# Kernel optimization log

Hardware: AMD Instinct MI355X
Metric: run time of the kernel (lower is better)

Reference implementation:

```python
import jax, jax.numpy as jnp
import numpy as np

WS = 4      # window size (hardcoded in original forward)
NH = 2      # num_head (module-level constant in original)


def _ln(x, g, b):
    mu = jnp.mean(x, axis=-1, keepdims=True)
    var = jnp.mean((x - mu) ** 2, axis=-1, keepdims=True)
    return (x - mu) * jax.lax.rsqrt(var + 1e-5) * g + b


def _img_to_win(img):
    # [B,H,W,D] -> [B, nW, WS*WS, D]  (matches F.unfold + reshape/transpose)
    B, H, W, D = img.shape
    s = H // WS
    x = img.reshape(B, s, WS, s, WS, D).transpose(0, 1, 3, 2, 4, 5)
    return x.reshape(B, s * s, WS * WS, D)


def _win_to_img(w):
    # [B, nW, WS*WS, D] -> [B,H,W,D]  (matches window2image)
    B, nW, P, D = w.shape
    s = int(np.sqrt(nW))
    x = w.reshape(B, s, s, WS, WS, D).transpose(0, 1, 3, 2, 4, 5)
    return x.reshape(B, s * WS, s * WS, D)


def _mhsa(x, wqkv, bqkv, wo, bo):
    # x: [B, S, D]; note: the original ignores additive_mask, so none is applied
    B, S, D = x.shape
    d = D // NH
    qkv = x @ wqkv.T + bqkv
    q, k, v = jnp.split(qkv, 3, axis=-1)
    q = q.reshape(B, S, NH, d).transpose(0, 2, 1, 3)
    k = k.reshape(B, S, NH, d).transpose(0, 2, 1, 3)
    v = v.reshape(B, S, NH, d).transpose(0, 2, 1, 3)
    p = jax.nn.softmax(jnp.einsum('bhqd,bhkd->bhqk', q, k) / np.sqrt(d).astype(np.float32), axis=-1)
    o = jnp.einsum('bhqk,bhkd->bhqd', p, v).transpose(0, 2, 1, 3).reshape(B, S, D)
    return o @ wo.T + bo


def _gelu(x):
    return jax.nn.gelu(x, approximate=False)


def setup_inputs() -> dict:
    key = jax.random.key(0)
    D = 128
    ks = jax.random.split(key, 16)
    w = lambda k, shp: (jax.random.normal(k, shp, dtype=jnp.float32) * 0.02)
    inp = {
        'x': jax.random.normal(ks[0], (8, 16384, D), dtype=jnp.float32),
        'ln1_g': jnp.ones((D,), jnp.float32), 'ln1_b': jnp.zeros((D,), jnp.float32),
        'ln2_g': jnp.ones((D,), jnp.float32), 'ln2_b': jnp.zeros((D,), jnp.float32),
        'ln3_g': jnp.ones((D,), jnp.float32), 'ln3_b': jnp.zeros((D,), jnp.float32),
        'ln4_g': jnp.ones((D,), jnp.float32), 'ln4_b': jnp.zeros((D,), jnp.float32),
        'qkv1_w': w(ks[1], (3 * D, D)), 'qkv1_b': jnp.zeros((3 * D,), jnp.float32),
        'out1_w': w(ks[2], (D, D)),     'out1_b': jnp.zeros((D,), jnp.float32),
        'qkv2_w': w(ks[3], (3 * D, D)), 'qkv2_b': jnp.zeros((3 * D,), jnp.float32),
        'out2_w': w(ks[4], (D, D)),     'out2_b': jnp.zeros((D,), jnp.float32),
        'mlp1_w1': w(ks[5], (4 * D, D)), 'mlp1_b1': jnp.zeros((4 * D,), jnp.float32),
        'mlp1_w2': w(ks[6], (D, 4 * D)), 'mlp1_b2': jnp.zeros((D,), jnp.float32),
        'mlp2_w1': w(ks[7], (4 * D, D)), 'mlp2_b1': jnp.zeros((4 * D,), jnp.float32),
        'mlp2_w2': w(ks[8], (D, 4 * D)), 'mlp2_b2': jnp.zeros((D,), jnp.float32),
    }
    return inp


def reference(x, ln1_g, ln1_b, ln2_g, ln2_b, ln3_g, ln3_b, ln4_g, ln4_b,
              qkv1_w, qkv1_b, out1_w, out1_b, qkv2_w, qkv2_b, out2_w, out2_b,
              mlp1_w1, mlp1_b1, mlp1_w2, mlp1_b2, mlp2_w1, mlp2_b1, mlp2_w2, mlp2_b2):
    B, N, D = x.shape
    H = int(np.sqrt(N))
    # --- W-MSA branch ---
    x1 = _ln(x, ln1_g, ln1_b)
    wins = _img_to_win(x1.reshape(B, H, H, D))            # [B,nW,P,D]
    nW, P = wins.shape[1], wins.shape[2]
    a1 = _mhsa(wins.reshape(B * nW, P, D), qkv1_w, qkv1_b, out1_w, out1_b)
    # original: input.long() -> truncate toward zero, detached; residual adds
    # window-order flattening (plain reshape, NOT window2image)
    res1 = jax.lax.stop_gradient(jnp.trunc(x)) + a1.reshape(B, N, D)
    h = _gelu(_ln(res1, ln2_g, ln2_b) @ mlp1_w1.T + mlp1_b1)
    h = _gelu(h @ mlp1_w2.T + mlp1_b2)
    out1 = h + res1
    # --- SW-MSA branch ---
    w2 = _ln(out1, ln3_g, ln3_b).reshape(B, nW, P, D)     # plain reshape (window order)
    img = jnp.roll(_win_to_img(w2), (-WS // 2, -WS // 2), axis=(1, 2))
    a2 = _mhsa(_img_to_win(img).reshape(B * nW, P, D), qkv2_w, qkv2_b, out2_w, out2_b)
    img2 = jnp.roll(_win_to_img(a2.reshape(B, nW, P, D)), (WS // 2, WS // 2), axis=(1, 2))
    res2 = out1 + _img_to_win(img2).reshape(B, N, D)      # plain reshape again
    h2 = _gelu(_ln(res2, ln4_g, ln4_b) @ mlp2_w1.T + mlp2_b1)
    h2 = _gelu(h2 @ mlp2_w2.T + mlp2_b2)
    out2 = h2 + res2
    return out2.reshape(B, nW, P, D)
```

## Files before the change

kernel.cpp:

```cpp
#include <hip/hip_runtime.h>
#include <hip/hip_bf16.h>
#include <string.h>


typedef unsigned short u16;
typedef unsigned int   u32;
typedef __attribute__((ext_vector_type(8))) short bf16x8;
typedef __attribute__((ext_vector_type(4))) float f32x4;

#define MFMA(a,b,c) __builtin_amdgcn_mfma_f32_16x16x32_bf16(a,b,c,0,0,0)

__device__ __forceinline__ u16 f2bf(float x) {
    __hip_bfloat16 h = __float2bfloat16(x);
    u16 r; memcpy(&r, &h, 2); return r;
}
__device__ __forceinline__ u32 pack2(float lo, float hi) {
    __hip_bfloat162 h = __float22bfloat162_rn(make_float2(lo, hi));
    u32 r; memcpy(&r, &h, 4); return r;
}
__device__ __forceinline__ float gelu_fast(float x) {
    float t = x * fmaf(x * x, 0.044715f, 1.0f);
    float e = __builtin_amdgcn_exp2f(-2.3022078f * t);
    return x * __builtin_amdgcn_rcpf(1.0f + e);
}
__device__ __forceinline__ bf16x8 ldsfrag(const u16* base, int byte) {
    return *(const bf16x8*)((const char*)base + byte);
}
__device__ __forceinline__ bf16x8 ldg8(const u16* __restrict__ p) {
    return *(const bf16x8*)p;
}
template <int BRANCH>
__device__ __forceinline__ int src_index(int wg, int tok) {
    int win = (wg << 2) + (tok >> 4), p = tok & 15;
    int r = ((win >> 5) << 2) | (p >> 2);
    int c = ((win & 31) << 2) | (p & 3);
    if (BRANCH == 1) return (r << 7) | c;
    int r2 = (r + 2) & 127, c2 = (c + 2) & 127;
    return ((((r2 >> 2) << 5) | (c2 >> 2)) << 4) | ((r2 & 3) << 2) | (c2 & 3);
}

__global__ __launch_bounds__(256)
void cvt_weights(const float* __restrict__ qkv1, const float* __restrict__ o1,
                 const float* __restrict__ w11,  const float* __restrict__ w12,
                 const float* __restrict__ qkv2, const float* __restrict__ o2,
                 const float* __restrict__ w21,  const float* __restrict__ w22,
                 u16* __restrict__ dst)
{
    int e = (blockIdx.x * 256 + threadIdx.x) * 8;
    const float* src; int off;
    if      (e < 49152)  { src = qkv1; off = 0; }
    else if (e < 65536)  { src = o1;   off = 49152; }
    else if (e < 131072) { src = w11;  off = 65536; }
    else if (e < 196608) { src = w12;  off = 131072; }
    else if (e < 245760) { src = qkv2; off = 196608; }
    else if (e < 262144) { src = o2;   off = 245760; }
    else if (e < 327680) { src = w21;  off = 262144; }
    else                 { src = w22;  off = 327680; }
    float4 a = *(const float4*)(src + (e - off));
    float4 b = *(const float4*)(src + (e - off) + 4);
    uint4 o;
    o.x = pack2(a.x, a.y); o.y = pack2(a.z, a.w);
    o.z = pack2(b.x, b.y); o.w = pack2(b.z, b.w);
    *(uint4*)(dst + e) = o;
}

template <int BRANCH>
__global__ __launch_bounds__(512, 4)
void swin_fused(const float* __restrict__ xin,
                const float* __restrict__ resin,
                float* __restrict__ resout,
                const float* __restrict__ lnA_g, const float* __restrict__ lnA_b,
                const float* __restrict__ lnB_g, const float* __restrict__ lnB_b,
                const u16* __restrict__ qkvw, const float* __restrict__ qkvb,
                const u16* __restrict__ ow,   const float* __restrict__ ob,
                const u16* __restrict__ w1,   const float* __restrict__ b1,
                const u16* __restrict__ w2,   const float* __restrict__ b2)
{
    __shared__ __align__(16) char smem[81920];
    u16*   xs   = (u16*)smem;
    u16*   qls  = (u16*)(smem + 16384);
    u16*   kls  = (u16*)(smem + 32768);
    u16*   vt   = (u16*)(smem + 49152);
    float* resf = (float*)(smem + 16384);
    u16*   h1   = (u16*)(smem + 49152);

    const int t  = threadIdx.x;
    const int wv = t >> 6, ln = t & 63, l15 = ln & 15, q4 = ln >> 4;
    const int bb = blockIdx.x >> 8, wg = blockIdx.x & 255;
    const int xa = (l15 & 7) << 4;
    const size_t gbase = (size_t)bb * 16384;

    {
        int token = t >> 3, part = t & 7;
        int nsrc = src_index<BRANCH>(wg, token);
        const float* src = xin + (gbase + nsrc) * 128;
        float v[16];
#pragma unroll
        for (int j = 0; j < 4; ++j)
            *(float4*)&v[j * 4] = *(const float4*)(src + part * 4 + 32 * j);
        float s = 0.f, s2 = 0.f;
#pragma unroll
        for (int i = 0; i < 16; ++i) { s += v[i]; s2 += v[i] * v[i]; }
        s  += __shfl_xor(s, 1, 8);  s  += __shfl_xor(s, 2, 8);  s  += __shfl_xor(s, 4, 8);
        s2 += __shfl_xor(s2, 1, 8); s2 += __shfl_xor(s2, 2, 8); s2 += __shfl_xor(s2, 4, 8);
        float mu = s * (1.f / 128.f);
        float rstd = rsqrtf(s2 * (1.f / 128.f) - mu * mu + 1e-5f);
        int xk = (token & 7) << 4;
#pragma unroll
        for (int j = 0; j < 4; ++j) {
            int d0 = part * 4 + 32 * j;
            float a0 = (v[j * 4 + 0] - mu) * rstd * lnA_g[d0]     + lnA_b[d0];
            float a1 = (v[j * 4 + 1] - mu) * rstd * lnA_g[d0 + 1] + lnA_b[d0 + 1];
            float a2 = (v[j * 4 + 2] - mu) * rstd * lnA_g[d0 + 2] + lnA_b[d0 + 2];
            float a3 = (v[j * 4 + 3] - mu) * rstd * lnA_g[d0 + 3] + lnA_b[d0 + 3];
            int byte = token * 256 + ((part * 8 + j * 64) ^ xk);
            *(uint2*)((char*)xs + byte) = make_uint2(pack2(a0, a1), pack2(a2, a3));
        }
        int row = t >> 2, base = row * 256 + 128 + (t & 3) * 32;
        uint4 z = {0, 0, 0, 0};
        *(uint4*)((char*)vt + base)      = z;
        *(uint4*)((char*)vt + base + 16) = z;
    }
    __syncthreads();

#pragma unroll 1
    for (int i = 0; i < 3; ++i) {
        int n0 = (wv * 3 + i) * 16;
        int part = n0 >> 7, c0 = n0 & 127;
        float bias = qkvb[n0 + l15];
        f32x4 acc[4];
#pragma unroll
        for (int mf = 0; mf < 4; ++mf) acc[mf] = (f32x4){bias, bias, bias, bias};
#pragma unroll
        for (int kf = 0; kf < 4; ++kf) {
            bf16x8 bfr = ldg8(qkvw + (size_t)(n0 + l15) * 128 + kf * 32 + q4 * 8);
#pragma unroll
            for (int mf = 0; mf < 4; ++mf) {
                bf16x8 afr = ldsfrag(xs, (mf * 16 + l15) * 256 + ((kf * 64 + q4 * 16) ^ xa));
                acc[mf] = MFMA(afr, bfr, acc[mf]);
            }
        }
        if (part < 2) {
            u16* dst = part ? kls : qls;
            float sc = part ? 1.f : 0.125f;
#pragma unroll
            for (int mf = 0; mf < 4; ++mf)
#pragma unroll
                for (int r = 0; r < 4; ++r) {
                    int tok = mf * 16 + q4 * 4 + r;
                    int byte = tok * 256 + ((2 * (c0 + l15)) ^ ((tok & 7) << 4));
                    dst[byte >> 1] = f2bf(acc[mf][r] * sc);
                }
        } else {
            int dh = c0 + l15, xr = (dh & 7) << 4;
#pragma unroll
            for (int mf = 0; mf < 4; ++mf) {
                int tok0 = mf * 16 + q4 * 4;
                u32 lo = pack2(acc[mf][0], acc[mf][1]);
                u32 hi = pack2(acc[mf][2], acc[mf][3]);
                int byte = dh * 256 + ((2 * tok0) ^ xr);
                *(uint2*)((char*)vt + byte) = make_uint2(lo, hi);
            }
        }
    }
    __syncthreads();

    f32x4 S;
    {
        int win = wv >> 1, h = wv & 1;
        f32x4 z = {0.f, 0.f, 0.f, 0.f};
        int tok = win * 16 + l15, xk = (tok & 7) << 4;
#pragma unroll
        for (int kf = 0; kf < 2; ++kf) {
            int byte = tok * 256 + ((h * 128 + kf * 64 + q4 * 16) ^ xk);
            bf16x8 aq = ldsfrag(qls, byte);
            bf16x8 bk = ldsfrag(kls, byte);
            z = MFMA(aq, bk, z);
        }
        S = z;
    }
    __syncthreads();

    {
        int win = wv >> 1, h = wv & 1;
#pragma unroll
        for (int r = 0; r < 4; ++r) {
            float v = S[r];
            float m = v;
            m = fmaxf(m, __shfl_xor(m, 1, 16)); m = fmaxf(m, __shfl_xor(m, 2, 16));
            m = fmaxf(m, __shfl_xor(m, 4, 16)); m = fmaxf(m, __shfl_xor(m, 8, 16));
            float e = __builtin_amdgcn_exp2f((v - m) * 1.44269504f);
            float sm = e;
            sm += __shfl_xor(sm, 1, 16); sm += __shfl_xor(sm, 2, 16);
            sm += __shfl_xor(sm, 4, 16); sm += __shfl_xor(sm, 8, 16);
            float p = e * __builtin_amdgcn_rcpf(sm);
            int tok = win * 16 + q4 * 4 + r, xk = (tok & 7) << 4;
            qls[(tok * 128 + ((h * 64 + l15 * 2)      ^ xk)) >> 1] = f2bf(p);
            qls[(tok * 128 + ((h * 64 + 32 + l15 * 2) ^ xk)) >> 1] = 0;
        }
    }
    __syncthreads();

    {
        int win = wv >> 1, h = wv & 1;
        int atok = win * 16 + l15;
        bf16x8 ap = ldsfrag(qls, atok * 128 + ((h * 64 + q4 * 16) ^ ((atok & 7) << 4)));
#pragma unroll
        for (int nf = 0; nf < 4; ++nf) {
            int dh = h * 64 + nf * 16 + l15;
            bf16x8 bv = ldsfrag(vt, dh * 256 + ((win * 32 + q4 * 16) ^ ((dh & 7) << 4)));
            f32x4 z = {0.f, 0.f, 0.f, 0.f};
            f32x4 o = MFMA(ap, bv, z);
#pragma unroll
            for (int r = 0; r < 4; ++r) {
                int tok = win * 16 + q4 * 4 + r;
                xs[(tok * 256 + ((2 * dh) ^ ((tok & 7) << 4))) >> 1] = f2bf(o[r]);
            }
        }
    }
    __syncthreads();

    {
        int n0 = wv * 16;
        float bias = ob[n0 + l15];
        f32x4 acc[4];
#pragma unroll
        for (int mf = 0; mf < 4; ++mf) acc[mf] = (f32x4){bias, bias, bias, bias};
#pragma unroll
        for (int kf = 0; kf < 4; ++kf) {
            bf16x8 bfr = ldg8(ow + (size_t)(n0 + l15) * 128 + kf * 32 + q4 * 8);
#pragma unroll
            for (int mf = 0; mf < 4; ++mf) {
                bf16x8 afr = ldsfrag(xs, (mf * 16 + l15) * 256 + ((kf * 64 + q4 * 16) ^ xa));
                acc[mf] = MFMA(afr, bfr, acc[mf]);
            }
        }
#pragma unroll
        for (int mf = 0; mf < 4; ++mf)
#pragma unroll
            for (int r = 0; r < 4; ++r) {
                int tok = mf * 16 + q4 * 4 + r;
                int nd = (BRANCH == 1) ? (wg * 64 + tok) : src_index<2>(wg, tok);
                float rv = resin[(gbase + nd) * 128 + n0 + l15];
                if (BRANCH == 1) rv = truncf(rv);
                int byte = tok * 512 + ((4 * (n0 + l15)) ^ ((tok & 7) << 4));
                *(float*)((char*)resf + byte) = rv + acc[mf][r];
            }
    }
    __syncthreads();

    {
        int token = t >> 3, part = t & 7;
        int xk = (token & 7) << 4;
        float v[16];
#pragma unroll
        for (int j = 0; j < 4; ++j)
            *(float4*)&v[j * 4] =
                *(const float4*)((char*)resf + token * 512 + ((part * 16 + j * 128) ^ xk));
        float s = 0.f, s2 = 0.f;
#pragma unroll
        for (int i = 0; i < 16; ++i) { s += v[i]; s2 += v[i] * v[i]; }
        s  += __shfl_xor(s, 1, 8);  s  += __shfl_xor(s, 2, 8);  s  += __shfl_xor(s, 4, 8);
        s2 += __shfl_xor(s2, 1, 8); s2 += __shfl_xor(s2, 2, 8); s2 += __shfl_xor(s2, 4, 8);
        float mu = s * (1.f / 128.f);
        float rstd = rsqrtf(s2 * (1.f / 128.f) - mu * mu + 1e-5f);
#pragma unroll
        for (int j = 0; j < 4; ++j) {
            int d0 = part * 4 + 32 * j;
            float a0 = (v[j * 4 + 0] - mu) * rstd * lnB_g[d0]     + lnB_b[d0];
            float a1 = (v[j * 4 + 1] - mu) * rstd * lnB_g[d0 + 1] + lnB_b[d0 + 1];
            float a2 = (v[j * 4 + 2] - mu) * rstd * lnB_g[d0 + 2] + lnB_b[d0 + 2];
            float a3 = (v[j * 4 + 3] - mu) * rstd * lnB_g[d0 + 3] + lnB_b[d0 + 3];
            int byte = token * 256 + ((part * 8 + j * 64) ^ xk);
            *(uint2*)((char*)xs + byte) = make_uint2(pack2(a0, a1), pack2(a2, a3));
        }
    }
    __syncthreads();

    const int nm = wv * 16;
    f32x4 acc2[4];
    {
        float bias = b2[nm + l15];
#pragma unroll
        for (int mf = 0; mf < 4; ++mf) acc2[mf] = (f32x4){bias, bias, bias, bias};
    }
#pragma unroll 1
    for (int c = 0; c < 4; ++c) {
        float bias = b1[c * 128 + nm + l15];
        f32x4 acc1[4];
#pragma unroll
        for (int mf = 0; mf < 4; ++mf) acc1[mf] = (f32x4){bias, bias, bias, bias};
#pragma unroll
        for (int kf = 0; kf < 4; ++kf) {
            bf16x8 bfr = ldg8(w1 + (size_t)(c * 128 + nm + l15) * 128 + kf * 32 + q4 * 8);
#pragma unroll
            for (int mf = 0; mf < 4; ++mf) {
                bf16x8 afr = ldsfrag(xs, (mf * 16 + l15) * 256 + ((kf * 64 + q4 * 16) ^ xa));
                acc1[mf] = MFMA(afr, bfr, acc1[mf]);
            }
        }
        __syncthreads();
#pragma unroll
        for (int mf = 0; mf < 4; ++mf)
#pragma unroll
            for (int r = 0; r < 4; ++r) {
                int tok = mf * 16 + q4 * 4 + r;
                h1[(tok * 256 + ((2 * (nm + l15)) ^ ((tok & 7) << 4))) >> 1] =
                    f2bf(gelu_fast(acc1[mf][r]));
            }
        __syncthreads();
#pragma unroll
        for (int kf = 0; kf < 4; ++kf) {
            bf16x8 bfr = ldg8(w2 + (size_t)(nm + l15) * 512 + c * 128 + kf * 32 + q4 * 8);
#pragma unroll
            for (int mf = 0; mf < 4; ++mf) {
                bf16x8 afr = ldsfrag(h1, (mf * 16 + l15) * 256 + ((kf * 64 + q4 * 16) ^ xa));
                acc2[mf] = MFMA(afr, bfr, acc2[mf]);
            }
        }
    }

#pragma unroll
    for (int mf = 0; mf < 4; ++mf)
#pragma unroll
        for (int r = 0; r < 4; ++r) {
            int tok = mf * 16 + q4 * 4 + r;
            int nd = (BRANCH == 1) ? (wg * 64 + tok) : src_index<2>(wg, tok);
            float res = *(const float*)((char*)resf +
                            tok * 512 + ((4 * (nm + l15)) ^ ((tok & 7) << 4)));
            resout[(gbase + nd) * 128 + nm + l15] = gelu_fast(acc2[mf][r]) + res;
        }
}

extern "C" void kernel_launch(void* const* d_in, const int* in_sizes, int n_in,
                              void* d_out, int out_size, void* d_ws, size_t ws_size,
                              hipStream_t stream) {
    (void)in_sizes; (void)n_in; (void)out_size; (void)ws_size;
    const float* x      = (const float*)d_in[0];
    const float* ln1_g  = (const float*)d_in[1];
    const float* ln1_b  = (const float*)d_in[2];
    const float* ln2_g  = (const float*)d_in[3];
    const float* ln2_b  = (const float*)d_in[4];
    const float* ln3_g  = (const float*)d_in[5];
    const float* ln3_b  = (const float*)d_in[6];
    const float* ln4_g  = (const float*)d_in[7];
    const float* ln4_b  = (const float*)d_in[8];
    const float* qkv1_w = (const float*)d_in[9];
    const float* qkv1_b = (const float*)d_in[10];
    const float* out1_w = (const float*)d_in[11];
    const float* out1_b = (const float*)d_in[12];
    const float* qkv2_w = (const float*)d_in[13];
    const float* qkv2_b = (const float*)d_in[14];
    const float* out2_w = (const float*)d_in[15];
    const float* out2_b = (const float*)d_in[16];
    const float* mlp1_w1 = (const float*)d_in[17];
    const float* mlp1_b1 = (const float*)d_in[18];
    const float* mlp1_w2 = (const float*)d_in[19];
    const float* mlp1_b2 = (const float*)d_in[20];
    const float* mlp2_w1 = (const float*)d_in[21];
    const float* mlp2_b1 = (const float*)d_in[22];
    const float* mlp2_w2 = (const float*)d_in[23];
    const float* mlp2_b2 = (const float*)d_in[24];

    u16* wb = (u16*)d_ws;
    u16* qkv1bf = wb + 0;
    u16* out1bf = wb + 49152;
    u16* m1w1bf = wb + 65536;
    u16* m1w2bf = wb + 131072;
    u16* qkv2bf = wb + 196608;
    u16* out2bf = wb + 245760;
    u16* m2w1bf = wb + 262144;
    u16* m2w2bf = wb + 327680;

    float* out = (float*)d_out;

    cvt_weights<<<dim3(192), dim3(256), 0, stream>>>(
        qkv1_w, out1_w, mlp1_w1, mlp1_w2, qkv2_w, out2_w, mlp2_w1, mlp2_w2, wb);

    swin_fused<1><<<dim3(2048), dim3(512), 0, stream>>>(
        x, x, out,
        ln1_g, ln1_b, ln2_g, ln2_b,
        qkv1bf, qkv1_b, out1bf, out1_b,
        m1w1bf, mlp1_b1, m1w2bf, mlp1_b2);

    swin_fused<2><<<dim3(2048), dim3(512), 0, stream>>>(
        out, out, out,
        ln3_g, ln3_b, ln4_g, ln4_b,
        qkv2bf, qkv2_b, out2bf, out2_b,
        m2w1bf, mlp2_b1, m2w2bf, mlp2_b2);
}
```

Measured before the change: 277.4 us.

## Halve block tile to 32 tokens with 4 waves and 2x2 MLP register tiles

Each workgroup now handles 2 windows (32 tokens) with 256 threads instead of 4 windows with 512 threads. LDS drops from 80KB to 40KB and the grid doubles, so more workgroups can be resident per CU and the tail is finer-grained. Each wave now computes 32 output columns over 32 tokens, and the MLP uses 2x2 fragment register tiles so each A fragment is reused across two B fragments. The trade-off is that every weight is read from global/L2 by twice as many blocks, raising weight traffic per token.

```diff
diff --git a/kernel.cpp b/kernel.cpp
--- a/kernel.cpp
+++ b/kernel.cpp
@@ -31,7 +31,7 @@
 }
 template <int BRANCH>
 __device__ __forceinline__ int src_index(int wg, int tok) {
-    int win = (wg << 2) + (tok >> 4), p = tok & 15;
+    int win = (wg << 1) + (tok >> 4), p = tok & 15;
     int r = ((win >> 5) << 2) | (p >> 2);
     int c = ((win & 31) << 2) | (p & 3);
     if (BRANCH == 1) return (r << 7) | c;
@@ -65,7 +65,7 @@
 }
 
 template <int BRANCH>
-__global__ __launch_bounds__(512, 4)
+__global__ __launch_bounds__(256, 4)
 void swin_fused(const float* __restrict__ xin,
                 const float* __restrict__ resin,
                 float* __restrict__ resout,
@@ -76,17 +76,17 @@
                 const u16* __restrict__ w1,   const float* __restrict__ b1,
                 const u16* __restrict__ w2,   const float* __restrict__ b2)
 {
-    __shared__ __align__(16) char smem[81920];
+    __shared__ __align__(16) char smem[40960];
     u16*   xs   = (u16*)smem;
-    u16*   qls  = (u16*)(smem + 16384);
-    u16*   kls  = (u16*)(smem + 32768);
-    u16*   vt   = (u16*)(smem + 49152);
-    float* resf = (float*)(smem + 16384);
-    u16*   h1   = (u16*)(smem + 49152);
+    u16*   qls  = (u16*)(smem + 8192);
+    u16*   kls  = (u16*)(smem + 16384);
+    u16*   vt   = (u16*)(smem + 24576);
+    float* resf = (float*)(smem + 8192);
+    u16*   h1   = (u16*)(smem + 24576);
 
     const int t  = threadIdx.x;
     const int wv = t >> 6, ln = t & 63, l15 = ln & 15, q4 = ln >> 4;
-    const int bb = blockIdx.x >> 8, wg = blockIdx.x & 255;
+    const int bb = blockIdx.x >> 9, wg = blockIdx.x & 511;
     const int xa = (l15 & 7) << 4;
     const size_t gbase = (size_t)bb * 16384;
 
@@ -116,26 +116,28 @@
             int byte = token * 256 + ((part * 8 + j * 64) ^ xk);
             *(uint2*)((char*)xs + byte) = make_uint2(pack2(a0, a1), pack2(a2, a3));
         }
-        int row = t >> 2, base = row * 256 + 128 + (t & 3) * 32;
+        int row = t >> 1, base = row * 128 + (t & 1) * 64;
         uint4 z = {0, 0, 0, 0};
         *(uint4*)((char*)vt + base)      = z;
         *(uint4*)((char*)vt + base + 16) = z;
+        *(uint4*)((char*)vt + base + 32) = z;
+        *(uint4*)((char*)vt + base + 48) = z;
     }
     __syncthreads();
 
 #pragma unroll 1
-    for (int i = 0; i < 3; ++i) {
-        int n0 = (wv * 3 + i) * 16;
+    for (int i = 0; i < 6; ++i) {
+        int n0 = (wv * 6 + i) * 16;
         int part = n0 >> 7, c0 = n0 & 127;
         float bias = qkvb[n0 + l15];
-        f32x4 acc[4];
-#pragma unroll
-        for (int mf = 0; mf < 4; ++mf) acc[mf] = (f32x4){bias, bias, bias, bias};
+        f32x4 acc[2];
+#pragma unroll
+        for (int mf = 0; mf < 2; ++mf) acc[mf] = (f32x4){bias, bias, bias, bias};
 #pragma unroll
         for (int kf = 0; kf < 4; ++kf) {
             bf16x8 bfr = ldg8(qkvw + (size_t)(n0 + l15) * 128 + kf * 32 + q4 * 8);
 #pragma unroll
-            for (int mf = 0; mf < 4; ++mf) {
+            for (int mf = 0; mf < 2; ++mf) {
                 bf16x8 afr = ldsfrag(xs, (mf * 16 + l15) * 256 + ((kf * 64 + q4 * 16) ^ xa));
                 acc[mf] = MFMA(afr, bfr, acc[mf]);
             }
@@ -144,7 +146,7 @@
             u16* dst = part ? kls : qls;
             float sc = part ? 1.f : 0.125f;
 #pragma unroll
-            for (int mf = 0; mf < 4; ++mf)
+            for (int mf = 0; mf < 2; ++mf)
 #pragma unroll
                 for (int r = 0; r < 4; ++r) {
                     int tok = mf * 16 + q4 * 4 + r;
@@ -154,11 +156,11 @@
         } else {
             int dh = c0 + l15, xr = (dh & 7) << 4;
 #pragma unroll
-            for (int mf = 0; mf < 4; ++mf) {
+            for (int mf = 0; mf < 2; ++mf) {
                 int tok0 = mf * 16 + q4 * 4;
                 u32 lo = pack2(acc[mf][0], acc[mf][1]);
                 u32 hi = pack2(acc[mf][2], acc[mf][3]);
-                int byte = dh * 256 + ((2 * tok0) ^ xr);
+                int byte = dh * 128 + ((2 * tok0) ^ xr);
                 *(uint2*)((char*)vt + byte) = make_uint2(lo, hi);
             }
         }
@@ -208,7 +210,7 @@
 #pragma unroll
         for (int nf = 0; nf < 4; ++nf) {
             int dh = h * 64 + nf * 16 + l15;
-            bf16x8 bv = ldsfrag(vt, dh * 256 + ((win * 32 + q4 * 16) ^ ((dh & 7) << 4)));
+            bf16x8 bv = ldsfrag(vt, dh * 128 + ((win * 32 + q4 * 16) ^ ((dh & 7) << 4)));
             f32x4 z = {0.f, 0.f, 0.f, 0.f};
             f32x4 o = MFMA(ap, bv, z);
 #pragma unroll
@@ -221,31 +223,35 @@
     __syncthreads();
 
     {
-        int n0 = wv * 16;
-        float bias = ob[n0 + l15];
-        f32x4 acc[4];
-#pragma unroll
-        for (int mf = 0; mf < 4; ++mf) acc[mf] = (f32x4){bias, bias, bias, bias};
-#pragma unroll
-        for (int kf = 0; kf < 4; ++kf) {
-            bf16x8 bfr = ldg8(ow + (size_t)(n0 + l15) * 128 + kf * 32 + q4 * 8);
-#pragma unroll
-            for (int mf = 0; mf < 4; ++mf) {
-                bf16x8 afr = ldsfrag(xs, (mf * 16 + l15) * 256 + ((kf * 64 + q4 * 16) ^ xa));
-                acc[mf] = MFMA(afr, bfr, acc[mf]);
-            }
-        }
-#pragma unroll
-        for (int mf = 0; mf < 4; ++mf)
-#pragma unroll
-            for (int r = 0; r < 4; ++r) {
-                int tok = mf * 16 + q4 * 4 + r;
-                int nd = (BRANCH == 1) ? (wg * 64 + tok) : src_index<2>(wg, tok);
-                float rv = resin[(gbase + nd) * 128 + n0 + l15];
-                if (BRANCH == 1) rv = truncf(rv);
-                int byte = tok * 512 + ((4 * (n0 + l15)) ^ ((tok & 7) << 4));
-                *(float*)((char*)resf + byte) = rv + acc[mf][r];
-            }
+        int n0 = wv * 32;
+#pragma unroll 1
+        for (int nf = 0; nf < 2; ++nf) {
+            int col0 = n0 + nf * 16;
+            float bias = ob[col0 + l15];
+            f32x4 acc[2];
+#pragma unroll
+            for (int mf = 0; mf < 2; ++mf) acc[mf] = (f32x4){bias, bias, bias, bias};
+#pragma unroll
+            for (int kf = 0; kf < 4; ++kf) {
+                bf16x8 bfr = ldg8(ow + (size_t)(col0 + l15) * 128 + kf * 32 + q4 * 8);
+#pragma unroll
+                for (int mf = 0; mf < 2; ++mf) {
+                    bf16x8 afr = ldsfrag(xs, (mf * 16 + l15) * 256 + ((kf * 64 + q4 * 16) ^ xa));
+                    acc[mf] = MFMA(afr, bfr, acc[mf]);
+                }
+            }
+#pragma unroll
+            for (int mf = 0; mf < 2; ++mf)
+#pragma unroll
+                for (int r = 0; r < 4; ++r) {
+                    int tok = mf * 16 + q4 * 4 + r;
+                    int nd = (BRANCH == 1) ? (wg * 32 + tok) : src_index<2>(wg, tok);
+                    float rv = resin[(gbase + nd) * 128 + col0 + l15];
+                    if (BRANCH == 1) rv = truncf(rv);
+                    int byte = tok * 512 + ((4 * (col0 + l15)) ^ ((tok & 7) << 4));
+                    *(float*)((char*)resf + byte) = rv + acc[mf][r];
+                }
+        }
     }
     __syncthreads();
 
@@ -277,59 +283,79 @@
     }
     __syncthreads();
 
-    const int nm = wv * 16;
-    f32x4 acc2[4];
-    {
-        float bias = b2[nm + l15];
-#pragma unroll
-        for (int mf = 0; mf < 4; ++mf) acc2[mf] = (f32x4){bias, bias, bias, bias};
+    const int nm = wv * 32;
+    f32x4 acc2[2][2];
+#pragma unroll
+    for (int nf = 0; nf < 2; ++nf) {
+        float bias = b2[nm + nf * 16 + l15];
+#pragma unroll
+        for (int mf = 0; mf < 2; ++mf) acc2[mf][nf] = (f32x4){bias, bias, bias, bias};
     }
 #pragma unroll 1
     for (int c = 0; c < 4; ++c) {
-        float bias = b1[c * 128 + nm + l15];
-        f32x4 acc1[4];
-#pragma unroll
-        for (int mf = 0; mf < 4; ++mf) acc1[mf] = (f32x4){bias, bias, bias, bias};
+        f32x4 acc1[2][2];
+#pragma unroll
+        for (int nf = 0; nf < 2; ++nf) {
+            float bias = b1[c * 128 + nm + nf * 16 + l15];
+#pragma unroll
+            for (int mf = 0; mf < 2; ++mf) acc1[mf][nf] = (f32x4){bias, bias, bias, bias};
+        }
 #pragma unroll
         for (int kf = 0; kf < 4; ++kf) {
-            bf16x8 bfr = ldg8(w1 + (size_t)(c * 128 + nm + l15) * 128 + kf * 32 + q4 * 8);
-#pragma unroll
-            for (int mf = 0; mf < 4; ++mf) {
-                bf16x8 afr = ldsfrag(xs, (mf * 16 + l15) * 256 + ((kf * 64 + q4 * 16) ^ xa));
-                acc1[mf] = MFMA(afr, bfr, acc1[mf]);
+            bf16x8 afr[2];
+#pragma unroll
+            for (int mf = 0; mf < 2; ++mf)
+                afr[mf] = ldsfrag(xs, (mf * 16 + l15) * 256 + ((kf * 64 + q4 * 16) ^ xa));
+#pragma unroll
+            for (int nf = 0; nf < 2; ++nf) {
+                bf16x8 bfr = ldg8(w1 + (size_t)(c * 128 + nm + nf * 16 + l15) * 128 + kf * 32 + q4 * 8);
+#pragma unroll
+                for (int mf = 0; mf < 2; ++mf) acc1[mf][nf] = MFMA(afr[mf], bfr, acc1[mf][nf]);
             }
         }
         __syncthreads();
 #pragma unroll
-        for (int mf = 0; mf < 4; ++mf)
+        for (int nf = 0; nf < 2; ++nf) {
+            int lc = nm + nf * 16 + l15;
+#pragma unroll
+            for (int mf = 0; mf < 2; ++mf)
+#pragma unroll
+                for (int r = 0; r < 4; ++r) {
+                    int tok = mf * 16 + q4 * 4 + r;
+                    h1[(tok * 256 + ((2 * lc) ^ ((tok & 7) << 4))) >> 1] =
+                        f2bf(gelu_fast(acc1[mf][nf][r]));
+                }
+        }
+        __syncthreads();
+#pragma unroll
+        for (int kf = 0; kf < 4; ++kf) {
+            bf16x8 afr[2];
+#pragma unroll
+            for (int mf = 0; mf < 2; ++mf)
+                afr[mf] = ldsfrag(h1, (mf * 16 + l15) * 256 + ((kf * 64 + q4 * 16) ^ xa));
+#pragma unroll
+            for (int nf = 0; nf < 2; ++nf) {
+                bf16x8 bfr = ldg8(w2 + (size_t)(nm + nf * 16 + l15) * 512 + c * 128 + kf * 32 + q4 * 8);
+#pragma unroll
+                for (int mf = 0; mf < 2; ++mf) acc2[mf][nf] = MFMA(afr[mf], bfr, acc2[mf][nf]);
+            }
+        }
+    }
+
+#pragma unroll
+    for (int nf = 0; nf < 2; ++nf) {
+        int col = nm + nf * 16 + l15;
+#pragma unroll
+        for (int mf = 0; mf < 2; ++mf)
 #pragma unroll
             for (int r = 0; r < 4; ++r) {
                 int tok = mf * 16 + q4 * 4 + r;
-                h1[(tok * 256 + ((2 * (nm + l15)) ^ ((tok & 7) << 4))) >> 1] =
-                    f2bf(gelu_fast(acc1[mf][r]));
-            }
-        __syncthreads();
-#pragma unroll
-        for (int kf = 0; kf < 4; ++kf) {
-            bf16x8 bfr = ldg8(w2 + (size_t)(nm + l15) * 512 + c * 128 + kf * 32 + q4 * 8);
-#pragma unroll
-            for (int mf = 0; mf < 4; ++mf) {
-                bf16x8 afr = ldsfrag(h1, (mf * 16 + l15) * 256 + ((kf * 64 + q4 * 16) ^ xa));
-                acc2[mf] = MFMA(afr, bfr, acc2[mf]);
-            }
-        }
-    }
-
-#pragma unroll
-    for (int mf = 0; mf < 4; ++mf)
-#pragma unroll
-        for (int r = 0; r < 4; ++r) {
-            int tok = mf * 16 + q4 * 4 + r;
-            int nd = (BRANCH == 1) ? (wg * 64 + tok) : src_index<2>(wg, tok);
-            float res = *(const float*)((char*)resf +
-                            tok * 512 + ((4 * (nm + l15)) ^ ((tok & 7) << 4)));
-            resout[(gbase + nd) * 128 + nm + l15] = gelu_fast(acc2[mf][r]) + res;
-        }
+                int nd = (BRANCH == 1) ? (wg * 32 + tok) : src_index<2>(wg, tok);
+                float res = *(const float*)((char*)resf +
+                                tok * 512 + ((4 * col) ^ ((tok & 7) << 4)));
+                resout[(gbase + nd) * 128 + col] = gelu_fast(acc2[mf][nf][r]) + res;
+            }
+    }
 }
 
 extern "C" void kernel_launch(void* const* d_in, const int* in_sizes, int n_in,
@@ -377,13 +403,13 @@
     cvt_weights<<<dim3(192), dim3(256), 0, stream>>>(
         qkv1_w, out1_w, mlp1_w1, mlp1_w2, qkv2_w, out2_w, mlp2_w1, mlp2_w2, wb);
 
-    swin_fused<1><<<dim3(2048), dim3(512), 0, stream>>>(
+    swin_fused<1><<<dim3(4096), dim3(256), 0, stream>>>(
         x, x, out,
         ln1_g, ln1_b, ln2_g, ln2_b,
         qkv1bf, qkv1_b, out1bf, out1_b,
         m1w1bf, mlp1_b1, m1w2bf, mlp1_b2);
 
-    swin_fused<2><<<dim3(2048), dim3(512), 0, stream>>>(
+    swin_fused<2><<<dim3(4096), dim3(256), 0, stream>>>(
         out, out, out,
         ln3_g, ln3_b, ln4_g, ln4_b,
         qkv2bf, qkv2_b, out2bf, out2_b,
```

Measured after the change: 407.5 us. 46.9% more time.
